# Kernel optimization log

Measured on AMD Instinct MI355X. Metric: run time of the kernel, lower is better.

Reference implementation:

```python
import jax, jax.numpy as jnp
import numpy as np

# NF4 (NormalFloat4) codebook from bitsandbytes
NF4 = jnp.array([
    -1.0, -0.6961928009986877, -0.5250730514526367, -0.39491748809814453,
    -0.28444138169288635, -0.18477343022823334, -0.09105003625154495, 0.0,
    0.07958029955625534, 0.16093020141124725, 0.24611230194568634,
    0.33791524171829224, 0.44070982933044434, 0.5626170039176941,
    0.7229568362236023, 1.0], dtype=jnp.float32)

BLOCK = 64          # bnb default quantization block size
RANK = 8
ALPHA = 16
SCALING = ALPHA / RANK


def setup_inputs() -> dict:
    key = jax.random.key(0)
    k = jax.random.split(key, 6)
    B, S, I, O = 4, 2048, 4096, 4096
    x = jax.random.normal(k[0], (B, S, I), dtype=jnp.float32)
    w_codes = jax.random.randint(k[1], (O, I), 0, 16, dtype=jnp.int32)
    absmax = jax.random.uniform(k[2], (O, I // BLOCK), dtype=jnp.float32)
    bias = jax.random.normal(k[3], (O,), dtype=jnp.float32)
    lora_A = jax.random.normal(k[4], (I, RANK), dtype=jnp.float32) / np.sqrt(I)
    lora_B = jax.random.normal(k[5], (RANK, O), dtype=jnp.float32)
    return {"x": x, "w_codes": w_codes, "absmax": absmax, "bias": bias,
            "lora_A": lora_A, "lora_B": lora_B}


def reference(x, w_codes, absmax, bias, lora_A, lora_B):
    O, I = w_codes.shape
    # NF4 dequantize: code lookup scaled by per-block absmax -> W [O, I]
    W = (NF4[w_codes].reshape(O, I // BLOCK, BLOCK) * absmax[:, :, None]).reshape(O, I)
    base = jnp.einsum('bsi,oi->bso', x, W) + bias
    # low-rank LoRA branch (dropout=0 -> identity)
    lora = ((x @ lora_A) @ lora_B) * SCALING
    return base + lora
```

## Files before the change

### kernel.cpp

```cpp
#include <hip/hip_runtime.h>
#include <hip/hip_bf16.h>
#include <stdint.h>


typedef __bf16 bf16x8 __attribute__((ext_vector_type(8)));
typedef float  f32x4  __attribute__((ext_vector_type(4)));
typedef unsigned short u16x8 __attribute__((ext_vector_type(8)));

__constant__ float NF4_TAB[16] = {
    -1.0f, -0.6961928009986877f, -0.5250730514526367f, -0.39491748809814453f,
    -0.28444138169288635f, -0.18477343022823334f, -0.09105003625154495f, 0.0f,
    0.07958029955625534f, 0.16093020141124725f, 0.24611230194568634f,
    0.33791524171829224f, 0.44070982933044434f, 0.5626170039176941f,
    0.7229568362236023f, 1.0f};

__device__ __forceinline__ unsigned short f2bf(float f) {
    unsigned int u = __float_as_uint(f);
    u += 0x7FFFu + ((u >> 16) & 1u);
    return (unsigned short)(u >> 16);
}

#define CVT_BLOCKS 4096
#define BLD_BLOCKS 2048

__global__ __launch_bounds__(256) void prep_kernel(
    const float* __restrict__ x, unsigned short* __restrict__ xb, int n8,
    const int* __restrict__ codes, const float* __restrict__ absmax,
    const float* __restrict__ lA, const float* __restrict__ lB,
    unsigned short* __restrict__ W, int O, int I, int nW8) {
    if ((int)blockIdx.x < CVT_BLOCKS) {
        const int base = blockIdx.x * 256 + threadIdx.x;
        const int stride = CVT_BLOCKS * 256;
#pragma unroll
        for (int k = 0; k < 4; ++k) {
            const int i = base + k * stride;
            if (i < n8) {
                const float4* p = (const float4*)x + (long)i * 2;
                float4 a = p[0], b = p[1];
                u16x8 o;
                o[0] = f2bf(a.x); o[1] = f2bf(a.y); o[2] = f2bf(a.z); o[3] = f2bf(a.w);
                o[4] = f2bf(b.x); o[5] = f2bf(b.y); o[6] = f2bf(b.z); o[7] = f2bf(b.w);
                *((u16x8*)xb + i) = o;
            }
        }
    } else {
        const int base = (blockIdx.x - CVT_BLOCKS) * 256 + threadIdx.x;
        const int stride = BLD_BLOCKS * 256;
        const int gpr = I >> 3;
#pragma unroll
        for (int k = 0; k < 4; ++k) {
            const int g8 = base + k * stride;
            if (g8 < nW8) {
                const int o  = g8 / gpr;
                const int i0 = (g8 - o * gpr) << 3;
                float bo[8];
#pragma unroll
                for (int r = 0; r < 8; ++r) bo[r] = lB[(long)r * O + o] * 2.0f;
                const long bse = (long)o * I + i0;
                const int4* cp = (const int4*)(codes + bse);
                int4 c0 = cp[0], c1 = cp[1];
                const float am = absmax[o * (I >> 6) + (i0 >> 6)];
                int cc[8] = {c0.x, c0.y, c0.z, c0.w, c1.x, c1.y, c1.z, c1.w};
                u16x8 ov;
#pragma unroll
                for (int j = 0; j < 8; ++j) {
                    const float4* ap = (const float4*)(lA + (long)(i0 + j) * 8);
                    float4 a0 = ap[0], a1 = ap[1];
                    float wv = NF4_TAB[cc[j] & 15] * am;
                    wv += a0.x * bo[0] + a0.y * bo[1] + a0.z * bo[2] + a0.w * bo[3]
                        + a1.x * bo[4] + a1.y * bo[5] + a1.z * bo[6] + a1.w * bo[7];
                    ov[j] = f2bf(wv);
                }
                *(u16x8*)(W + bse) = ov;
            }
        }
    }
}

#define BM 256
#define BN 256
#define BK 64

#define GLOAD16(g, s) __builtin_amdgcn_global_load_lds(                     \
    (const __attribute__((address_space(1))) void*)(g),                     \
    (__attribute__((address_space(3))) void*)(s), 16, 0, 0)

#define STAGE(ptr, ldsbase) do {                                            \
    GLOAD16((ptr), (char*)(ldsbase) + ldsW);                                \
    GLOAD16((ptr) + SK, (char*)(ldsbase) + 8192 + ldsW); } while (0)

#define BAR() do { asm volatile("" ::: "memory");                           \
    __builtin_amdgcn_s_barrier(); asm volatile("" ::: "memory"); } while (0)

#define MFMA_QUAD(H, KQ, BREG)                                              \
    _Pragma("unroll") for (int mi = 0; mi < 4; ++mi)                        \
    _Pragma("unroll") for (int ni = 0; ni < 2; ++ni) {                      \
        acc[H][KQ][mi][ni] = __builtin_amdgcn_mfma_f32_16x16x32_bf16(       \
            a[mi][0], BREG[ni][0], acc[H][KQ][mi][ni], 0, 0, 0);            \
        acc[H][KQ][mi][ni] = __builtin_amdgcn_mfma_f32_16x16x32_bf16(       \
            a[mi][1], BREG[ni][1], acc[H][KQ][mi][ni], 0, 0, 0); }

__global__ __launch_bounds__(512, 2) void gemm_kernel(
    const unsigned short* __restrict__ A,
    const unsigned short* __restrict__ Bm,
    const float* __restrict__ bias,
    float* __restrict__ out, int M, int N, int K, int gx, int gy) {
    __shared__ char lds[65536];

    int bx, by;
    {
        const int bid = blockIdx.x;
        if ((gx & 7) == 0 && (gy & 7) == 0 && ((gx >> 3) * (gy >> 3)) == 8) {
            const int xcd = bid & 7, loc = bid >> 3;
            const int cxs = gx >> 3;
            const int cr = xcd / cxs, cc = xcd - cr * cxs;
            by = cr * 8 + (loc >> 3);
            bx = cc * 8 + (loc & 7);
        } else if (((gx * gy) & 7) == 0) {
            const int q = (gx * gy) >> 3;
            const int id = (bid & 7) * q + (bid >> 3);
            bx = id % gx; by = id / gx;
        } else { bx = bid % gx; by = bid / gx; }
    }

    const int t = threadIdx.x;
    const int w = t >> 6, l = t & 63;
    const int wr = w >> 2, wc = w & 3;
    const long mB = (long)by * BM;
    const long nB = (long)bx * BN;
    const int NT = K / BK;

    const int sRow = w * 8 + (l >> 3);
    const int sCol = ((l & 7) ^ (l >> 3)) << 3;
    const int ldsW = w * 1024;
    const long SK = 64L * K;
    const long HK = 128L * K;
    const unsigned short* gA = A  + (mB + sRow) * K + sCol;
    const unsigned short* gB = Bm + (nB + sRow) * K + sCol;

    const unsigned short* pA1 = gA + HK;
    const unsigned short* pA0 = gA + BK;
    const unsigned short* pB0 = gB + BK;
    const unsigned short* pB1 = gB + HK + BK;

    const int fr = l & 15;
    const int aoff0 = fr * 128 + ((((l >> 4)) ^ (l & 7)) << 4);
    const int aoff1 = fr * 128 + (((4 + (l >> 4)) ^ (l & 7)) << 4);

    f32x4 acc[2][2][4][2];
#pragma unroll
    for (int h = 0; h < 2; ++h)
#pragma unroll
        for (int k = 0; k < 2; ++k)
#pragma unroll
            for (int mi = 0; mi < 4; ++mi)
#pragma unroll
                for (int ni = 0; ni < 2; ++ni)
                    acc[h][k][mi][ni] = (f32x4){0.f, 0.f, 0.f, 0.f};

    STAGE(gA,      lds + 0);
    STAGE(gB,      lds + 32768);
    STAGE(gB + HK, lds + 49152);
    asm volatile("s_waitcnt vmcnt(0)" ::: "memory");
    BAR();

    bf16x8 a[4][2], b0[2][2], b1[2][2];
    const char* Ab = lds + wr * 8192;
    const char* Bb = lds + 32768 + wc * 4096;

    for (int g = 0; g < NT; ++g) {
        const bool st = (g + 1 < NT);

#pragma unroll
        for (int mi = 0; mi < 4; ++mi) {
            a[mi][0] = *(const bf16x8*)(Ab + mi * 2048 + aoff0);
            a[mi][1] = *(const bf16x8*)(Ab + mi * 2048 + aoff1);
        }
#pragma unroll
        for (int ni = 0; ni < 2; ++ni) {
            b0[ni][0] = *(const bf16x8*)(Bb + ni * 2048 + aoff0);
            b0[ni][1] = *(const bf16x8*)(Bb + ni * 2048 + aoff1);
            b1[ni][0] = *(const bf16x8*)(Bb + 16384 + ni * 2048 + aoff0);
            b1[ni][1] = *(const bf16x8*)(Bb + 16384 + ni * 2048 + aoff1);
        }
        STAGE(pA1, lds + 16384);
        __builtin_amdgcn_s_setprio(1);
        MFMA_QUAD(0, 0, b0);
        MFMA_QUAD(0, 1, b1);
        __builtin_amdgcn_s_setprio(0);
        asm volatile("s_waitcnt lgkmcnt(0)" ::: "memory");
        asm volatile("s_waitcnt vmcnt(0)" ::: "memory");
        BAR();

#pragma unroll
        for (int mi = 0; mi < 4; ++mi) {
            a[mi][0] = *(const bf16x8*)(Ab + 16384 + mi * 2048 + aoff0);
            a[mi][1] = *(const bf16x8*)(Ab + 16384 + mi * 2048 + aoff1);
        }
        if (st) {
            STAGE(pA0, lds + 0);
            STAGE(pB0, lds + 32768);
            STAGE(pB1, lds + 49152);
        }
        __builtin_amdgcn_s_setprio(1);
        MFMA_QUAD(1, 0, b0);
        MFMA_QUAD(1, 1, b1);
        __builtin_amdgcn_s_setprio(0);
        asm volatile("s_waitcnt lgkmcnt(0)" ::: "memory");
        asm volatile("s_waitcnt vmcnt(0)" ::: "memory");
        BAR();

        pA1 += BK; pA0 += BK; pB0 += BK; pB1 += BK;
    }

    const int r4 = (l >> 4) * 4;
#pragma unroll
    for (int kq = 0; kq < 2; ++kq) {
        float bs[2];
#pragma unroll
        for (int ni = 0; ni < 2; ++ni)
            bs[ni] = bias[nB + kq * 128 + wc * 32 + ni * 16 + fr];
#pragma unroll
        for (int h = 0; h < 2; ++h)
#pragma unroll
            for (int mi = 0; mi < 4; ++mi)
#pragma unroll
                for (int r = 0; r < 4; ++r) {
                    long row = mB + h * 128 + wr * 64 + mi * 16 + r4 + r;
                    float* op = out + row * N + nB + kq * 128 + wc * 32 + fr;
#pragma unroll
                    for (int ni = 0; ni < 2; ++ni)
                        op[ni * 16] = acc[h][kq][mi][ni][r] + bs[ni];
                }
    }
}

__global__ void naive_kernel(const float* __restrict__ x, const int* __restrict__ codes,
                             const float* __restrict__ absmax, const float* __restrict__ bias,
                             const float* __restrict__ lA, const float* __restrict__ lB,
                             float* __restrict__ out, int M, int I, int O) {
    long idx = (long)blockIdx.x * 256 + threadIdx.x;
    if (idx >= (long)M * O) return;
    int o = (int)(idx % O);
    long m = idx / O;
    const float* xr = x + m * I;
    const int* cr = codes + (long)o * I;
    const float* ar = absmax + (long)o * (I >> 6);
    float acc = 0.f;
    float la[8] = {0, 0, 0, 0, 0, 0, 0, 0};
    for (int i = 0; i < I; ++i) {
        float xv = xr[i];
        acc += xv * NF4_TAB[cr[i] & 15] * ar[i >> 6];
        const float* av = lA + (long)i * 8;
#pragma unroll
        for (int r = 0; r < 8; ++r) la[r] += xv * av[r];
    }
    float lv = 0.f;
#pragma unroll
    for (int r = 0; r < 8; ++r) lv += la[r] * lB[(long)r * O + o];
    out[idx] = acc + bias[o] + 2.0f * lv;
}

extern "C" void kernel_launch(void* const* d_in, const int* in_sizes, int n_in,
                              void* d_out, int out_size, void* d_ws, size_t ws_size,
                              hipStream_t stream) {
    const float* x      = (const float*)d_in[0];
    const int*   codes  = (const int*)d_in[1];
    const float* absmax = (const float*)d_in[2];
    const float* bias   = (const float*)d_in[3];
    const float* lA     = (const float*)d_in[4];
    const float* lB     = (const float*)d_in[5];
    float* out = (float*)d_out;

    const int I = in_sizes[4] / 8;
    const int O = in_sizes[3];
    const int M = in_sizes[0] / I;
    const int K = I;

    const size_t need = (size_t)M * K * 2 + (size_t)O * K * 2;
    if (ws_size < need || (M % BM) || (O % BN) || (K % 2048) || (K / BK) < 2) {
        long tot = (long)M * O;
        naive_kernel<<<(int)((tot + 255) / 256), 256, 0, stream>>>(
            x, codes, absmax, bias, lA, lB, out, M, I, O);
        return;
    }

    unsigned short* xb = (unsigned short*)d_ws;
    unsigned short* wb = xb + (size_t)M * K;

    const int n8  = (M * K) / 8;
    const int nW8 = (O * K) / 8;
    prep_kernel<<<CVT_BLOCKS + BLD_BLOCKS, 256, 0, stream>>>(
        x, xb, n8, codes, absmax, lA, lB, wb, O, K, nW8);
    const int gx = O / BN, gy = M / BM;
    gemm_kernel<<<gx * gy, 512, 0, stream>>>(xb, wb, bias, out, M, O, K, gx, gy);
}
```

Baseline: 353.9 us.

## Double-buffer LDS tiles to prefetch next K-step during MFMA

Switches the GEMM main loop from a single 64KB LDS buffer, with two barriers per K-iteration, to two 64KB buffers. All four sub-tiles for the next iteration are staged into the alternate buffer at the top of the loop, and only one barrier per iteration remains. The B-fragment reads are split so MFMAs can start after the first half loads. This doubles LDS to 128KB per block, which likely rules out the two blocks per CU that launch_bounds(512,2) asks for and so lowers occupancy.

New measurement: 356.6 us. Within noise of the previous version (+0.8%).

```diff
diff --git a/kernel.cpp b/kernel.cpp
--- a/kernel.cpp
+++ b/kernel.cpp
@@ -105,7 +105,7 @@
     const unsigned short* __restrict__ Bm,
     const float* __restrict__ bias,
     float* __restrict__ out, int M, int N, int K, int gx, int gy) {
-    __shared__ char lds[65536];
+    __shared__ char lds[2][65536];
 
     int bx, by;
     {
@@ -138,8 +138,8 @@
     const unsigned short* gA = A  + (mB + sRow) * K + sCol;
     const unsigned short* gB = Bm + (nB + sRow) * K + sCol;
 
-    const unsigned short* pA1 = gA + HK;
     const unsigned short* pA0 = gA + BK;
+    const unsigned short* pA1 = gA + HK + BK;
     const unsigned short* pB0 = gB + BK;
     const unsigned short* pB1 = gB + HK + BK;
 
@@ -158,18 +158,28 @@
                 for (int ni = 0; ni < 2; ++ni)
                     acc[h][k][mi][ni] = (f32x4){0.f, 0.f, 0.f, 0.f};
 
-    STAGE(gA,      lds + 0);
-    STAGE(gB,      lds + 32768);
-    STAGE(gB + HK, lds + 49152);
+    STAGE(gA,      lds[0] + 0);
+    STAGE(gA + HK, lds[0] + 16384);
+    STAGE(gB,      lds[0] + 32768);
+    STAGE(gB + HK, lds[0] + 49152);
     asm volatile("s_waitcnt vmcnt(0)" ::: "memory");
     BAR();
 
     bf16x8 a[4][2], b0[2][2], b1[2][2];
-    const char* Ab = lds + wr * 8192;
-    const char* Bb = lds + 32768 + wc * 4096;
 
     for (int g = 0; g < NT; ++g) {
+        char* cur = lds[g & 1];
+        char* nxt = lds[(g & 1) ^ 1];
+        const char* Ab = cur + wr * 8192;
+        const char* Bb = cur + 32768 + wc * 4096;
         const bool st = (g + 1 < NT);
+
+        if (st) {
+            STAGE(pA0, nxt + 0);
+            STAGE(pA1, nxt + 16384);
+            STAGE(pB0, nxt + 32768);
+            STAGE(pB1, nxt + 49152);
+        }
 
 #pragma unroll
         for (int mi = 0; mi < 4; ++mi) {
@@ -180,37 +190,34 @@
         for (int ni = 0; ni < 2; ++ni) {
             b0[ni][0] = *(const bf16x8*)(Bb + ni * 2048 + aoff0);
             b0[ni][1] = *(const bf16x8*)(Bb + ni * 2048 + aoff1);
+        }
+        __builtin_amdgcn_s_setprio(1);
+        MFMA_QUAD(0, 0, b0);
+        __builtin_amdgcn_s_setprio(0);
+
+#pragma unroll
+        for (int ni = 0; ni < 2; ++ni) {
             b1[ni][0] = *(const bf16x8*)(Bb + 16384 + ni * 2048 + aoff0);
             b1[ni][1] = *(const bf16x8*)(Bb + 16384 + ni * 2048 + aoff1);
         }
-        STAGE(pA1, lds + 16384);
         __builtin_amdgcn_s_setprio(1);
-        MFMA_QUAD(0, 0, b0);
         MFMA_QUAD(0, 1, b1);
         __builtin_amdgcn_s_setprio(0);
-        asm volatile("s_waitcnt lgkmcnt(0)" ::: "memory");
-        asm volatile("s_waitcnt vmcnt(0)" ::: "memory");
-        BAR();
 
 #pragma unroll
         for (int mi = 0; mi < 4; ++mi) {
             a[mi][0] = *(const bf16x8*)(Ab + 16384 + mi * 2048 + aoff0);
             a[mi][1] = *(const bf16x8*)(Ab + 16384 + mi * 2048 + aoff1);
-        }
-        if (st) {
-            STAGE(pA0, lds + 0);
-            STAGE(pB0, lds + 32768);
-            STAGE(pB1, lds + 49152);
         }
         __builtin_amdgcn_s_setprio(1);
         MFMA_QUAD(1, 0, b0);
         MFMA_QUAD(1, 1, b1);
         __builtin_amdgcn_s_setprio(0);
-        asm volatile("s_waitcnt lgkmcnt(0)" ::: "memory");
+
         asm volatile("s_waitcnt vmcnt(0)" ::: "memory");
         BAR();
 
-        pA1 += BK; pA0 += BK; pB0 += BK; pB1 += BK;
+        pA0 += BK; pA1 += BK; pB0 += BK; pB1 += BK;
     }
 
     const int r4 = (l >> 4) * 4;
```
